# Kernel tuning notes

Hardware: AMD Instinct MI355X
Metric: run time of the kernel (lower is better)

## Reference

```python
import jax, jax.numpy as jnp
import numpy as np

EPS = 1e-5


def _conv1x1(x, w, b):
    # x: (B,C,H,W), w: (O,C), b: (O,)
    return jnp.einsum('bchw,oc->bohw', x, w) + b[None, :, None, None]


def setup_inputs() -> dict:
    key = jax.random.key(0)
    ks = jax.random.split(key, 12)
    C, Ci = 512, 256
    B, H, W = 4, 64, 64
    s_in = 1.0 / np.sqrt(C)
    s_ci = 1.0 / np.sqrt(Ci)
    return {
        'x': jax.random.normal(ks[0], (B, C, H, W), dtype=jnp.float32),
        'g_w': jax.random.normal(ks[1], (Ci, C), dtype=jnp.float32) * s_in,
        'g_b': jax.random.normal(ks[2], (Ci,), dtype=jnp.float32) * 0.01,
        'theta_w': jax.random.normal(ks[3], (Ci, C), dtype=jnp.float32) * s_in,
        'theta_b': jax.random.normal(ks[4], (Ci,), dtype=jnp.float32) * 0.01,
        'phi_w': jax.random.normal(ks[5], (Ci, C), dtype=jnp.float32) * s_in,
        'phi_b': jax.random.normal(ks[6], (Ci,), dtype=jnp.float32) * 0.01,
        'W_w': jax.random.normal(ks[7], (C, Ci), dtype=jnp.float32) * s_ci,
        'W_b': jax.random.normal(ks[8], (C,), dtype=jnp.float32) * 0.01,
        'bn_gamma': jax.random.normal(ks[9], (C,), dtype=jnp.float32) * 0.1,
        'bn_beta': jax.random.normal(ks[10], (C,), dtype=jnp.float32) * 0.01,
    }


def reference(x, g_w, g_b, theta_w, theta_b, phi_w, phi_b, W_w, W_b, bn_gamma, bn_beta):
    B, C, H, W = x.shape
    Ci = g_w.shape[0]
    HW = H * W
    # 1x1-conv projections -> token form
    g = _conv1x1(x, g_w, g_b).reshape(B, Ci, HW).transpose(0, 2, 1)        # (B,HW,Ci)
    theta = _conv1x1(x, theta_w, theta_b).reshape(B, Ci, HW).transpose(0, 2, 1)  # (B,HW,Ci)
    phi = _conv1x1(x, phi_w, phi_b).reshape(B, Ci, HW)                      # (B,Ci,HW)
    # dense HWxHW attention, scaled by sqrt(inter_channels)
    pairwise = jnp.einsum('bnc,bcm->bnm', theta, phi) / jnp.sqrt(jnp.float32(Ci))
    attn = jax.nn.softmax(pairwise, axis=-1)
    y = jnp.einsum('bnm,bmc->bnc', attn, g)                                 # (B,HW,Ci)
    y = y.transpose(0, 2, 1).reshape(B, Ci, H, W)
    # output 1x1 conv + BatchNorm2d (training-mode batch statistics)
    z = _conv1x1(y, W_w, W_b)
    mean = jnp.mean(z, axis=(0, 2, 3), keepdims=True)
    var = jnp.var(z, axis=(0, 2, 3), keepdims=True)
    z = bn_gamma[None, :, None, None] * (z - mean) * jax.lax.rsqrt(var + EPS) + bn_beta[None, :, None, None]
    return z + x
```

## Files before the change

kernel.cpp:

```cpp
#include <hip/hip_runtime.h>

typedef unsigned short u16;
typedef __attribute__((ext_vector_type(4))) u16 u16x4;
typedef __attribute__((ext_vector_type(8))) u16 u16x8;
typedef __attribute__((ext_vector_type(8))) short s16x8;
typedef __attribute__((ext_vector_type(4))) float f32x4;

#define B_  4
#define C_  512
#define CI_ 256
#define HW_ 4096

static __device__ __forceinline__ u16 f2bf(float f) {
  unsigned u = __float_as_uint(f);
  return (u16)((u + 0x7FFFu + ((u >> 16) & 1u)) >> 16);
}
static __device__ __forceinline__ float bf2f(u16 h) {
  return __uint_as_float(((unsigned)h) << 16);
}

static __device__ __forceinline__ f32x4 mfma16(s16x8 a, s16x8 b, f32x4 c) {
  return __builtin_amdgcn_mfma_f32_16x16x32_bf16(a, b, c, 0, 0, 0);
}

typedef __attribute__((address_space(3))) unsigned int as3_u32;
typedef const __attribute__((address_space(1))) unsigned int as1_u32;
static __device__ __forceinline__ void gload16(const u16* g, u16* l) {
  __builtin_amdgcn_global_load_lds((as1_u32*)g, (as3_u32*)l, 16, 0, 0);
}

__global__ __launch_bounds__(256) void k0_wcvt(
    const float* __restrict__ wg, const float* __restrict__ wt,
    const float* __restrict__ wp, const float* __restrict__ Ww,
    u16* __restrict__ wB, u16* __restrict__ WwB)
{
  int idx = (blockIdx.x * 256 + threadIdx.x) * 8;
  const float* src;
  u16* dst;
  if (idx < 393216) {
    int r = idx >> 17;
    src = (r == 0 ? wg : r == 1 ? wt : wp) + (idx & 131071);
    dst = wB + idx;
  } else {
    src = Ww + (idx - 393216);
    dst = WwB + (idx - 393216);
  }
  float4 v0 = *reinterpret_cast<const float4*>(src);
  float4 v1 = *reinterpret_cast<const float4*>(src + 4);
  u16x8 h;
  h[0] = f2bf(v0.x); h[1] = f2bf(v0.y); h[2] = f2bf(v0.z); h[3] = f2bf(v0.w);
  h[4] = f2bf(v1.x); h[5] = f2bf(v1.y); h[6] = f2bf(v1.z); h[7] = f2bf(v1.w);
  *reinterpret_cast<u16x8*>(dst) = h;
}

__global__ __launch_bounds__(256) void k0_xt(
    const float* __restrict__ x, u16* __restrict__ xT, int b0)
{
  __shared__ u16 lds[64][72];
  const int tid = threadIdx.x;
  const int n0 = blockIdx.x * 64, c0 = blockIdx.y * 64;
  const int bl = blockIdx.z;
  const int b = b0 + bl;
  const int nc = (tid & 15) * 4;
#pragma unroll
  for (int i = 0; i < 4; ++i) {
    int cr = (tid >> 4) + i * 16;
    float4 v = *reinterpret_cast<const float4*>(
        &x[((size_t)(b * C_ + c0 + cr)) * HW_ + n0 + nc]);
    u16x4 h; h[0] = f2bf(v.x); h[1] = f2bf(v.y); h[2] = f2bf(v.z); h[3] = f2bf(v.w);
    *reinterpret_cast<u16x4*>(&lds[cr][nc]) = h;
  }
  __syncthreads();
  const int n = tid & 63, cg = tid >> 6;
  u16x8 o0, o1;
#pragma unroll
  for (int j = 0; j < 8; ++j) { o0[j] = lds[cg * 16 + j][n]; o1[j] = lds[cg * 16 + 8 + j][n]; }
  size_t dstb = ((size_t)bl * HW_ + n0 + n) * C_ + c0 + cg * 16;
  *reinterpret_cast<u16x8*>(&xT[dstb])     = o0;
  *reinterpret_cast<u16x8*>(&xT[dstb + 8]) = o1;
}

__global__ __launch_bounds__(256) void k1_proj(
    const u16* __restrict__ wB, const u16* __restrict__ xT,
    const float* __restrict__ bg, const float* __restrict__ bt, const float* __restrict__ bp,
    u16* __restrict__ g_s, u16* __restrict__ thetaT, u16* __restrict__ phiT, int half)
{
  extern __shared__ u16 sm1[];
  const int tid = threadIdx.x;
  const int lane = tid & 63, wid = tid >> 6;
  const int wm = wid >> 1, wn = wid & 1;
  const int l15 = lane & 15, g4 = lane >> 4;

  const int bid = blockIdx.x;
  const int r12 = bid % 12;
  const int nt = bid / 12;
  const int mt = r12 >> 1;
  const int bl = r12 & 1;
  const int b = half * 2 + bl;
  const int m0 = mt * 128, n0g = nt * 128;
  const int p = mt >> 1;

  const u16* xb = xT + (size_t)bl * HW_ * C_;

  const int srow = tid >> 2, sch = tid & 3;
  const u16* a_src = wB + (size_t)(m0 + srow) * C_ + sch * 8;
  const u16* b_src = xb + (size_t)(n0g + srow) * C_ + sch * 8;

  f32x4 acc[4][4] = {};

  auto stage1 = [&](int buf, int ks) {
    u16* d = sm1 + buf * 8192;
#pragma unroll
    for (int i = 0; i < 2; ++i) {
      gload16(a_src + (size_t)(i * 64) * C_ + ks * 32, d + (tid + i * 256) * 8);
      gload16(b_src + (size_t)(i * 64) * C_ + ks * 32, d + 4096 + (tid + i * 256) * 8);
    }
  };
  auto compute1 = [&](int buf) {
    const u16* A = sm1 + buf * 8192;
    const u16* Bt = A + 4096;
    s16x8 afr[4], bfr[4];
#pragma unroll
    for (int mf = 0; mf < 4; ++mf)
      afr[mf] = *reinterpret_cast<const s16x8*>(&A[(wm * 64 + mf * 16 + l15) * 32 + g4 * 8]);
#pragma unroll
    for (int nf = 0; nf < 4; ++nf)
      bfr[nf] = *reinterpret_cast<const s16x8*>(&Bt[(wn * 64 + nf * 16 + l15) * 32 + g4 * 8]);
#pragma unroll
    for (int mf = 0; mf < 4; ++mf)
#pragma unroll
      for (int nf = 0; nf < 4; ++nf)
        acc[mf][nf] = mfma16(afr[mf], bfr[nf], acc[mf][nf]);
  };

  stage1(0, 0); stage1(1, 1);
  int cur = 0;
#pragma unroll 1
  for (int ks = 0; ks < 15; ++ks) {
    asm volatile("s_waitcnt vmcnt(4)" ::: "memory");
    __builtin_amdgcn_s_barrier();
    compute1(cur);
    if (ks < 14) { int nb = cur + 2; if (nb >= 3) nb -= 3; stage1(nb, ks + 2); }
    cur = (cur == 2) ? 0 : cur + 1;
  }
  asm volatile("s_waitcnt vmcnt(0)" ::: "memory");
  __builtin_amdgcn_s_barrier();
  compute1(cur);
  __syncthreads();

  const float* bias = (p == 0) ? bg : (p == 1) ? bt : bp;
  const int cib = (mt & 1) * 128;
#pragma unroll
  for (int mf = 0; mf < 4; ++mf)
#pragma unroll
    for (int r = 0; r < 4; ++r) {
      float bv = bias[cib + wm * 64 + mf * 16 + g4 * 4 + r];
#pragma unroll
      for (int nf = 0; nf < 4; ++nf) acc[mf][nf][r] += bv;
    }

  if (p == 0) {
    u16* lds_t = sm1;
#pragma unroll
    for (int mf = 0; mf < 4; ++mf)
#pragma unroll
      for (int nf = 0; nf < 4; ++nf)
#pragma unroll
        for (int r = 0; r < 4; ++r)
          lds_t[(wm * 64 + mf * 16 + g4 * 4 + r) * 136 + wn * 64 + nf * 16 + l15] =
              f2bf(acc[mf][nf][r]);
    __syncthreads();
    const int m = tid >> 1, hh = tid & 1;
    size_t dst = ((size_t)b * CI_ + cib + m) * HW_ + n0g + hh * 64;
#pragma unroll
    for (int j = 0; j < 8; ++j)
      *reinterpret_cast<u16x8*>(&g_s[dst + j * 8]) =
          *reinterpret_cast<const u16x8*>(&lds_t[m * 136 + hh * 64 + j * 8]);
  } else {
    u16* outp = (p == 1) ? thetaT : phiT;
#pragma unroll
    for (int mf = 0; mf < 4; ++mf)
#pragma unroll
      for (int nf = 0; nf < 4; ++nf) {
        u16x4 h;
#pragma unroll
        for (int r = 0; r < 4; ++r) h[r] = f2bf(acc[mf][nf][r]);
        int n = n0g + wn * 64 + nf * 16 + l15;
        *reinterpret_cast<u16x4*>(
            &outp[((size_t)b * HW_ + n) * CI_ + cib + wm * 64 + mf * 16 + g4 * 4]) = h;
      }
  }
}

#define OFF_PHI  0
#define OFF_G    16384
#define OFF_P    32768
#define OFF_LP   35072

__global__ __launch_bounds__(256, 2) void k3_fused(
    const u16* __restrict__ thetaT, const u16* __restrict__ phiT,
    const u16* __restrict__ g_s, u16* __restrict__ y)
{
  extern __shared__ u16 smem[];
  float* Lp = (float*)(smem + OFF_LP);
  float* iL = Lp + 128;

  const int tid = threadIdx.x;
  const int lane = tid & 63, w = tid >> 6;
  const int l15 = lane & 15, g4 = lane >> 4;

  const int bid = blockIdx.x;
  const int xcd = bid & 7, slot = bid >> 3;
  const int b  = xcd >> 1;
  const int n0 = ((xcd & 1) * 64 + slot) * 32;

  const int ms = w;
  const int cq = w;

  const u16* thb = thetaT + (size_t)b * HW_ * CI_;
  const u16* phb = phiT   + (size_t)b * HW_ * CI_;
  const u16* gsb = g_s    + (size_t)b * CI_ * HW_;

  s16x8 thfr[2][8];
#pragma unroll
  for (int nf = 0; nf < 2; ++nf)
#pragma unroll
    for (int cs = 0; cs < 8; ++cs)
      thfr[nf][cs] = *reinterpret_cast<const s16x8*>(
          &thb[(size_t)(n0 + nf * 16 + l15) * CI_ + cs * 32 + g4 * 8]);

  const int prow = tid >> 5, pj = tid & 31;
  const int grow = tid >> 3, gj = tid & 7;
  const u16* ph_src = phb + (size_t)prow * CI_ + ((pj ^ (prow & 7)) * 8);
  const u16* g_src  = gsb + (size_t)grow * HW_ + ((gj ^ (grow & 7)) * 8);
  const int ph_do = prow * 256 + pj * 8;
  const int g_do  = grow * 64 + gj * 8;

  auto stage_phi = [&](int mt) {
#pragma unroll
    for (int i = 0; i < 8; ++i)
      gload16(ph_src + (size_t)(mt + i * 8) * CI_, smem + OFF_PHI + ph_do + i * 2048);
  };
  auto stage_g = [&](int mt) {
#pragma unroll
    for (int i = 0; i < 8; ++i)
      gload16(g_src + mt + (size_t)i * 32 * HW_, smem + OFF_G + g_do + i * 2048);
  };

  f32x4 oacc[2][4] = {};
  float psum[2] = {0.f, 0.f};

  auto qk_it = [&]() {
    const u16* phc = smem + OFF_PHI;
    u16* pb = smem + OFF_P;
    f32x4 acc[2] = {};
    __builtin_amdgcn_s_setprio(1);
#pragma unroll
    for (int cs = 0; cs < 8; ++cs) {
      s16x8 a = *reinterpret_cast<const s16x8*>(
          &phc[(ms * 16 + l15) * 256 + (((cs * 4 + g4) ^ (l15 & 7)) * 8)]);
      acc[0] = mfma16(a, thfr[0][cs], acc[0]);
      acc[1] = mfma16(a, thfr[1][cs], acc[1]);
    }
    __builtin_amdgcn_s_setprio(0);
#pragma unroll
    for (int nf = 0; nf < 2; ++nf) {
      u16x4 pk;
#pragma unroll
      for (int r = 0; r < 4; ++r) {
        float e = __expf(acc[nf][r] * 0.0625f);
        psum[nf] += e;
        pk[r] = f2bf(e);
      }
      *reinterpret_cast<u16x4*>(&pb[(nf * 16 + l15) * 72 + ms * 16 + g4 * 4]) = pk;
    }
  };
  auto pv_it = [&]() {
    const u16* pb = smem + OFF_P;
    const u16* gC = smem + OFF_G;
    __builtin_amdgcn_s_setprio(1);
#pragma unroll
    for (int mk = 0; mk < 2; ++mk) {
      s16x8 pa[2];
#pragma unroll
      for (int nf = 0; nf < 2; ++nf)
        pa[nf] = *reinterpret_cast<const s16x8*>(
            &pb[(nf * 16 + l15) * 72 + mk * 32 + g4 * 8]);
#pragma unroll
      for (int cf = 0; cf < 4; ++cf) {
        int crow = cq * 64 + cf * 16 + l15;
        s16x8 bb = *reinterpret_cast<const s16x8*>(
            &gC[crow * 64 + (((mk * 4 + g4) ^ (crow & 7)) * 8)]);
        oacc[0][cf] = mfma16(pa[0], bb, oacc[0][cf]);
        oacc[1][cf] = mfma16(pa[1], bb, oacc[1][cf]);
      }
    }
    __builtin_amdgcn_s_setprio(0);
  };

  stage_phi(0);
  __syncthreads();

#pragma unroll 1
  for (int it = 0; it < 64; ++it) {
    stage_g(it * 64);
    qk_it();
    __syncthreads();
    if (it < 63) stage_phi((it + 1) * 64);
    pv_it();
    __syncthreads();
  }

#pragma unroll
  for (int nf = 0; nf < 2; ++nf) {
    psum[nf] += __shfl_xor(psum[nf], 16);
    psum[nf] += __shfl_xor(psum[nf], 32);
  }
  if (lane < 16) {
    Lp[w * 32 + lane]      = psum[0];
    Lp[w * 32 + 16 + lane] = psum[1];
  }
  __syncthreads();
  if (tid < 32) iL[tid] = 1.0f / (Lp[tid] + Lp[32 + tid] + Lp[64 + tid] + Lp[96 + tid]);
  __syncthreads();

  u16* yb = y + ((size_t)b * HW_ + n0) * CI_;
#pragma unroll
  for (int nf = 0; nf < 2; ++nf)
#pragma unroll
    for (int r = 0; r < 4; ++r) {
      int nl = nf * 16 + g4 * 4 + r;
      float il = iL[nl];
#pragma unroll
      for (int cf = 0; cf < 4; ++cf)
        yb[(size_t)nl * CI_ + cq * 64 + cf * 16 + l15] = f2bf(oacc[nf][cf][r] * il);
    }
}

__global__ __launch_bounds__(256) void k4_wconv(
    const u16* __restrict__ WwB, const u16* __restrict__ y, const float* __restrict__ Wb,
    u16* __restrict__ z, float* __restrict__ zsum, float* __restrict__ zsq)
{
  extern __shared__ u16 sm4[];
  __shared__ float lds_ps[2][128][2];
  const int tid = threadIdx.x;
  const int lane = tid & 63, wid = tid >> 6;
  const int wm = wid >> 1, wn = wid & 1;
  const int l15 = lane & 15, g4 = lane >> 4;

  const int bid = blockIdx.x;
  const int xcd = bid & 7, slot = bid >> 3;
  const int b = xcd >> 1, half = xcd & 1;
  const int mt = slot & 3;
  const int nt = half * 16 + (slot >> 2);
  const int o0 = mt * 128, n0g = nt * 128;

  const int srow = tid >> 2, sch = tid & 3;
  const u16* a_src = WwB + (size_t)(o0 + srow) * CI_ + sch * 8;
  const u16* b_src = y + ((size_t)(b * HW_ + n0g + srow)) * CI_ + sch * 8;

  f32x4 acc[4][4] = {};

  auto stage4 = [&](int buf, int ks) {
    u16* d = sm4 + buf * 8192;
#pragma unroll
    for (int i = 0; i < 2; ++i) {
      gload16(a_src + (size_t)(i * 64) * CI_ + ks * 32, d + (tid + i * 256) * 8);
      gload16(b_src + (size_t)(i * 64) * CI_ + ks * 32, d + 4096 + (tid + i * 256) * 8);
    }
  };
  auto compute4 = [&](int buf) {
    const u16* A = sm4 + buf * 8192;
    const u16* Bt = A + 4096;
    s16x8 afr[4], bfr[4];
#pragma unroll
    for (int mf = 0; mf < 4; ++mf)
      afr[mf] = *reinterpret_cast<const s16x8*>(&A[(wm * 64 + mf * 16 + l15) * 32 + g4 * 8]);
#pragma unroll
    for (int nf = 0; nf < 4; ++nf)
      bfr[nf] = *reinterpret_cast<const s16x8*>(&Bt[(wn * 64 + nf * 16 + l15) * 32 + g4 * 8]);
#pragma unroll
    for (int mf = 0; mf < 4; ++mf)
#pragma unroll
      for (int nf = 0; nf < 4; ++nf)
        acc[mf][nf] = mfma16(afr[mf], bfr[nf], acc[mf][nf]);
  };

  stage4(0, 0); stage4(1, 1);
  int cur = 0;
#pragma unroll 1
  for (int ks = 0; ks < 7; ++ks) {
    asm volatile("s_waitcnt vmcnt(4)" ::: "memory");
    __builtin_amdgcn_s_barrier();
    compute4(cur);
    if (ks < 6) { int nb = cur + 2; if (nb >= 3) nb -= 3; stage4(nb, ks + 2); }
    cur = (cur == 2) ? 0 : cur + 1;
  }
  asm volatile("s_waitcnt vmcnt(0)" ::: "memory");
  __builtin_amdgcn_s_barrier();
  compute4(cur);
  __syncthreads();

  u16* lds_t = sm4;
#pragma unroll
  for (int mf = 0; mf < 4; ++mf)
#pragma unroll
    for (int r = 0; r < 4; ++r) {
      const int ol = wm * 64 + mf * 16 + g4 * 4 + r;
      float wb = Wb[o0 + ol];
      float s = 0.f, q = 0.f;
#pragma unroll
      for (int nf = 0; nf < 4; ++nf) {
        float zv = acc[mf][nf][r] + wb;
        s += zv; q += zv * zv;
        lds_t[ol * 136 + wn * 64 + nf * 16 + l15] = f2bf(zv);
      }
      s += __shfl_xor(s, 1); s += __shfl_xor(s, 2); s += __shfl_xor(s, 4); s += __shfl_xor(s, 8);
      q += __shfl_xor(q, 1); q += __shfl_xor(q, 2); q += __shfl_xor(q, 4); q += __shfl_xor(q, 8);
      if (l15 == 0) { lds_ps[wn][ol][0] = s; lds_ps[wn][ol][1] = q; }
    }
  __syncthreads();
  {
    const int m = tid >> 1, hh = tid & 1;
    size_t dst = ((size_t)(b * C_ + o0 + m)) * HW_ + n0g + hh * 64;
#pragma unroll
    for (int j = 0; j < 8; ++j)
      *reinterpret_cast<u16x8*>(&z[dst + j * 8]) =
          *reinterpret_cast<const u16x8*>(&lds_t[m * 136 + hh * 64 + j * 8]);
  }
  if (tid < 128) {
    int col = b * 32 + nt;
    zsum[(size_t)(o0 + tid) * 128 + col] = lds_ps[0][tid][0] + lds_ps[1][tid][0];
    zsq [(size_t)(o0 + tid) * 128 + col] = lds_ps[0][tid][1] + lds_ps[1][tid][1];
  }
}

__global__ void k5_bnstat(const float* __restrict__ zsum, const float* __restrict__ zsq,
                          const float* __restrict__ gamma, const float* __restrict__ beta,
                          float* __restrict__ bns, float* __restrict__ bnb)
{
  int ch = blockIdx.x * 256 + threadIdx.x;
  if (ch >= C_) return;
  float s = 0.f, q = 0.f;
  for (int i = 0; i < 128; ++i) { s += zsum[(size_t)ch * 128 + i]; q += zsq[(size_t)ch * 128 + i]; }
  const float inv_n = 1.0f / (B_ * HW_);
  float mean = s * inv_n;
  float var  = q * inv_n - mean * mean;
  float sc = gamma[ch] * rsqrtf(var + 1e-5f);
  bns[ch] = sc;
  bnb[ch] = beta[ch] - mean * sc;
}

__global__ __launch_bounds__(256) void k6_final(
    const u16* __restrict__ z, const float* __restrict__ x,
    const float* __restrict__ bns, const float* __restrict__ bnb,
    float* __restrict__ out)
{
  size_t i = ((size_t)blockIdx.x * 256 + threadIdx.x) * 8;
  int ch = (int)((i >> 12) & 511);
  float sc = bns[ch], sh = bnb[ch];
  u16x8 zv = *reinterpret_cast<const u16x8*>(&z[i]);
  float4 x0 = *reinterpret_cast<const float4*>(&x[i]);
  float4 x1 = *reinterpret_cast<const float4*>(&x[i + 4]);
  float4 o0, o1;
  o0.x = bf2f(zv[0]) * sc + sh + x0.x;
  o0.y = bf2f(zv[1]) * sc + sh + x0.y;
  o0.z = bf2f(zv[2]) * sc + sh + x0.z;
  o0.w = bf2f(zv[3]) * sc + sh + x0.w;
  o1.x = bf2f(zv[4]) * sc + sh + x1.x;
  o1.y = bf2f(zv[5]) * sc + sh + x1.y;
  o1.z = bf2f(zv[6]) * sc + sh + x1.z;
  o1.w = bf2f(zv[7]) * sc + sh + x1.w;
  *reinterpret_cast<float4*>(&out[i])     = o0;
  *reinterpret_cast<float4*>(&out[i + 4]) = o1;
}

extern "C" void kernel_launch(void* const* d_in, const int* in_sizes, int n_in,
                              void* d_out, int out_size, void* d_ws, size_t ws_size,
                              hipStream_t stream)
{
  (void)in_sizes; (void)n_in; (void)out_size; (void)ws_size;
  const float* x    = (const float*)d_in[0];
  const float* g_w  = (const float*)d_in[1];
  const float* g_b  = (const float*)d_in[2];
  const float* t_w  = (const float*)d_in[3];
  const float* t_b  = (const float*)d_in[4];
  const float* p_w  = (const float*)d_in[5];
  const float* p_b  = (const float*)d_in[6];
  const float* W_w  = (const float*)d_in[7];
  const float* W_b  = (const float*)d_in[8];
  const float* bng  = (const float*)d_in[9];
  const float* bnb_ = (const float*)d_in[10];

  char* ws = (char*)d_ws;
  const size_t M8 = (size_t)8 << 20;
  u16*   xT     = (u16*)(ws + 0);
  u16*   y      = (u16*)(ws + 0);
  u16*   thetaT = (u16*)(ws + M8);
  u16*   phiT   = (u16*)(ws + 2 * M8);
  u16*   g_s    = (u16*)(ws + 3 * M8);
  u16*   zbf    = (u16*)(ws + M8);
  float* zsum   = (float*)(ws + 3 * M8);
  float* zsq    = (float*)(ws + 3 * M8 + 262144);
  float* bnsV   = (float*)(ws + 3 * M8 + 524288);
  float* bnbV   = (float*)(ws + 3 * M8 + 526336);
  u16*   wB     = (u16*)(ws + 4 * M8);
  u16*   WwB    = (u16*)(ws + 4 * M8 + 786432);
  float* out    = (float*)d_out;

  const int k1_lds = 49152;
  const int k3_lds = 70784;
  const int k4_lds = 49152;
  hipFuncSetAttribute(reinterpret_cast<const void*>(k1_proj),
                      hipFuncAttributeMaxDynamicSharedMemorySize, k1_lds);
  hipFuncSetAttribute(reinterpret_cast<const void*>(k3_fused),
                      hipFuncAttributeMaxDynamicSharedMemorySize, k3_lds);
  hipFuncSetAttribute(reinterpret_cast<const void*>(k4_wconv),
                      hipFuncAttributeMaxDynamicSharedMemorySize, k4_lds);

  hipLaunchKernelGGL(k0_wcvt, dim3(256), dim3(256), 0, stream,
                     g_w, t_w, p_w, W_w, wB, WwB);
  for (int half = 0; half < 2; ++half) {
    hipLaunchKernelGGL(k0_xt, dim3(64, 8, 2), dim3(256), 0, stream, x, xT, half * 2);
    hipLaunchKernelGGL(k1_proj, dim3(384), dim3(256), k1_lds, stream,
                       wB, xT, g_b, t_b, p_b, g_s, thetaT, phiT, half);
  }
  hipLaunchKernelGGL(k3_fused, dim3(512), dim3(256), k3_lds, stream,
                     thetaT, phiT, g_s, y);
  hipLaunchKernelGGL(k4_wconv, dim3(512), dim3(256), k4_lds, stream,
                     WwB, y, W_b, zbf, zsum, zsq);
  hipLaunchKernelGGL(k5_bnstat, dim3(2), dim3(256), 0, stream,
                     zsum, zsq, bng, bnb_, bnsV, bnbV);
  hipLaunchKernelGGL(k6_final, dim3(4096), dim3(256), 0, stream,
                     zbf, x, bnsV, bnbV, out);
}
```

Before: 201.6 us.

## Load phi fragments directly into registers with double buffering instead of LDS staging

Result: slower. 283.5 us (+40.6%).

```diff
diff --git a/kernel.cpp b/kernel.cpp
--- a/kernel.cpp
+++ b/kernel.cpp
@@ -192,10 +192,9 @@
   }
 }
 
-#define OFF_PHI  0
-#define OFF_G    16384
-#define OFF_P    32768
-#define OFF_LP   35072
+#define OFF_G    0
+#define OFF_P    16384
+#define OFF_LP   18688
 
 __global__ __launch_bounds__(256, 2) void k3_fused(
     const u16* __restrict__ thetaT, const u16* __restrict__ phiT,
@@ -229,38 +228,35 @@
       thfr[nf][cs] = *reinterpret_cast<const s16x8*>(
           &thb[(size_t)(n0 + nf * 16 + l15) * CI_ + cs * 32 + g4 * 8]);
 
-  const int prow = tid >> 5, pj = tid & 31;
   const int grow = tid >> 3, gj = tid & 7;
-  const u16* ph_src = phb + (size_t)prow * CI_ + ((pj ^ (prow & 7)) * 8);
   const u16* g_src  = gsb + (size_t)grow * HW_ + ((gj ^ (grow & 7)) * 8);
-  const int ph_do = prow * 256 + pj * 8;
   const int g_do  = grow * 64 + gj * 8;
 
-  auto stage_phi = [&](int mt) {
-#pragma unroll
-    for (int i = 0; i < 8; ++i)
-      gload16(ph_src + (size_t)(mt + i * 8) * CI_, smem + OFF_PHI + ph_do + i * 2048);
-  };
   auto stage_g = [&](int mt) {
 #pragma unroll
     for (int i = 0; i < 8; ++i)
       gload16(g_src + mt + (size_t)i * 32 * HW_, smem + OFF_G + g_do + i * 2048);
   };
 
+  const u16* ph_lane = phb + ((size_t)(ms * 16 + l15)) * CI_ + g4 * 8;
+  auto load_phi = [&](s16x8* ph, int mt) {
+    const u16* src = ph_lane + (size_t)mt * CI_;
+#pragma unroll
+    for (int cs = 0; cs < 8; ++cs)
+      ph[cs] = *reinterpret_cast<const s16x8*>(&src[cs * 32]);
+  };
+
   f32x4 oacc[2][4] = {};
   float psum[2] = {0.f, 0.f};
 
-  auto qk_it = [&]() {
-    const u16* phc = smem + OFF_PHI;
+  auto qk_it = [&](const s16x8* ph) {
     u16* pb = smem + OFF_P;
     f32x4 acc[2] = {};
     __builtin_amdgcn_s_setprio(1);
 #pragma unroll
     for (int cs = 0; cs < 8; ++cs) {
-      s16x8 a = *reinterpret_cast<const s16x8*>(
-          &phc[(ms * 16 + l15) * 256 + (((cs * 4 + g4) ^ (l15 & 7)) * 8)]);
-      acc[0] = mfma16(a, thfr[0][cs], acc[0]);
-      acc[1] = mfma16(a, thfr[1][cs], acc[1]);
+      acc[0] = mfma16(ph[cs], thfr[0][cs], acc[0]);
+      acc[1] = mfma16(ph[cs], thfr[1][cs], acc[1]);
     }
     __builtin_amdgcn_s_setprio(0);
 #pragma unroll
@@ -298,15 +294,22 @@
     __builtin_amdgcn_s_setprio(0);
   };
 
-  stage_phi(0);
-  __syncthreads();
+  s16x8 phiA[8], phiB[8];
+
+  load_phi(phiA, 0);
 
 #pragma unroll 1
-  for (int it = 0; it < 64; ++it) {
+  for (int it = 0; it < 64; it += 2) {
+    load_phi(phiB, (it + 1) * 64);
     stage_g(it * 64);
-    qk_it();
+    qk_it(phiA);
     __syncthreads();
-    if (it < 63) stage_phi((it + 1) * 64);
+    pv_it();
+    __syncthreads();
+    if (it + 2 < 64) load_phi(phiA, (it + 2) * 64);
+    stage_g((it + 1) * 64);
+    qk_it(phiB);
+    __syncthreads();
     pv_it();
     __syncthreads();
   }
@@ -509,7 +512,7 @@
   float* out    = (float*)d_out;
 
   const int k1_lds = 49152;
-  const int k3_lds = 70784;
+  const int k3_lds = 38016;
   const int k4_lds = 49152;
   hipFuncSetAttribute(reinterpret_cast<const void*>(k1_proj),
                       hipFuncAttributeMaxDynamicSharedMemorySize, k1_lds);
```

## Retile fused attention kernel to 64-row blocks with 32x32 bf16 MFMA

Applied to the files above, without the earlier changes.

Result: faster. 187.5 us, median of 2 (-7.0%).

```diff
diff --git a/kernel.cpp b/kernel.cpp
--- a/kernel.cpp
+++ b/kernel.cpp
@@ -5,6 +5,7 @@
 typedef __attribute__((ext_vector_type(8))) u16 u16x8;
 typedef __attribute__((ext_vector_type(8))) short s16x8;
 typedef __attribute__((ext_vector_type(4))) float f32x4;
+typedef __attribute__((ext_vector_type(16))) float f32x16;
 
 #define B_  4
 #define C_  512
@@ -21,6 +22,9 @@
 
 static __device__ __forceinline__ f32x4 mfma16(s16x8 a, s16x8 b, f32x4 c) {
   return __builtin_amdgcn_mfma_f32_16x16x32_bf16(a, b, c, 0, 0, 0);
+}
+static __device__ __forceinline__ f32x16 mfma32(s16x8 a, s16x8 b, f32x16 c) {
+  return __builtin_amdgcn_mfma_f32_32x32x16_bf16(a, b, c, 0, 0, 0);
 }
 
 typedef __attribute__((address_space(3))) unsigned int as3_u32;
@@ -193,106 +197,103 @@
 }
 
 #define OFF_PHI  0
-#define OFF_G    16384
-#define OFF_P    32768
-#define OFF_LP   35072
-
-__global__ __launch_bounds__(256, 2) void k3_fused(
+#define OFF_G    32768
+#define OFF_P    65536
+#define OFF_LP   73728
+
+__global__ __launch_bounds__(512, 2) void k3_fused(
     const u16* __restrict__ thetaT, const u16* __restrict__ phiT,
     const u16* __restrict__ g_s, u16* __restrict__ y)
 {
   extern __shared__ u16 smem[];
   float* Lp = (float*)(smem + OFF_LP);
-  float* iL = Lp + 128;
+  float* iL = Lp + 256;
 
   const int tid = threadIdx.x;
   const int lane = tid & 63, w = tid >> 6;
-  const int l15 = lane & 15, g4 = lane >> 4;
+  const int l31 = lane & 31, h = lane >> 5;
+  const int l15 = lane & 15;
 
   const int bid = blockIdx.x;
   const int xcd = bid & 7, slot = bid >> 3;
   const int b  = xcd >> 1;
-  const int n0 = ((xcd & 1) * 64 + slot) * 32;
-
-  const int ms = w;
-  const int cq = w;
+  const int n0 = ((xcd & 1) * 32 + slot) * 64;
+
+  const int mh = w >> 1, nh = w & 1;
+  const int cq = w >> 1, nh2 = w & 1;
 
   const u16* thb = thetaT + (size_t)b * HW_ * CI_;
   const u16* phb = phiT   + (size_t)b * HW_ * CI_;
   const u16* gsb = g_s    + (size_t)b * CI_ * HW_;
 
-  s16x8 thfr[2][8];
-#pragma unroll
-  for (int nf = 0; nf < 2; ++nf)
-#pragma unroll
-    for (int cs = 0; cs < 8; ++cs)
-      thfr[nf][cs] = *reinterpret_cast<const s16x8*>(
-          &thb[(size_t)(n0 + nf * 16 + l15) * CI_ + cs * 32 + g4 * 8]);
+  s16x8 thfr[16];
+#pragma unroll
+  for (int cs = 0; cs < 16; ++cs)
+    thfr[cs] = *reinterpret_cast<const s16x8*>(
+        &thb[(size_t)(n0 + nh * 32 + l31) * CI_ + cs * 16 + h * 8]);
 
   const int prow = tid >> 5, pj = tid & 31;
-  const int grow = tid >> 3, gj = tid & 7;
-  const u16* ph_src = phb + (size_t)prow * CI_ + ((pj ^ (prow & 7)) * 8);
-  const u16* g_src  = gsb + (size_t)grow * HW_ + ((gj ^ (grow & 7)) * 8);
+  const int grow = tid >> 4, gj = tid & 15;
+  const u16* ph_src = phb + (size_t)prow * CI_ + ((pj ^ prow) * 8);
+  const u16* g_src  = gsb + (size_t)grow * HW_ + ((gj ^ (grow & 15)) * 8);
   const int ph_do = prow * 256 + pj * 8;
-  const int g_do  = grow * 64 + gj * 8;
+  const int g_do  = grow * 128 + gj * 8;
 
   auto stage_phi = [&](int mt) {
 #pragma unroll
     for (int i = 0; i < 8; ++i)
-      gload16(ph_src + (size_t)(mt + i * 8) * CI_, smem + OFF_PHI + ph_do + i * 2048);
+      gload16(ph_src + (size_t)(mt + i * 16) * CI_, smem + OFF_PHI + ph_do + i * 4096);
   };
   auto stage_g = [&](int mt) {
 #pragma unroll
     for (int i = 0; i < 8; ++i)
-      gload16(g_src + mt + (size_t)i * 32 * HW_, smem + OFF_G + g_do + i * 2048);
-  };
-
-  f32x4 oacc[2][4] = {};
-  float psum[2] = {0.f, 0.f};
+      gload16(g_src + mt + (size_t)(i * 32) * HW_, smem + OFF_G + g_do + i * 4096);
+  };
+
+  f32x16 oacc[2] = {};
+  float psum = 0.f;
 
   auto qk_it = [&]() {
     const u16* phc = smem + OFF_PHI;
     u16* pb = smem + OFF_P;
-    f32x4 acc[2] = {};
+    f32x16 acc = {};
     __builtin_amdgcn_s_setprio(1);
 #pragma unroll
-    for (int cs = 0; cs < 8; ++cs) {
+    for (int cs = 0; cs < 16; ++cs) {
       s16x8 a = *reinterpret_cast<const s16x8*>(
-          &phc[(ms * 16 + l15) * 256 + (((cs * 4 + g4) ^ (l15 & 7)) * 8)]);
-      acc[0] = mfma16(a, thfr[0][cs], acc[0]);
-      acc[1] = mfma16(a, thfr[1][cs], acc[1]);
+          &phc[(mh * 32 + l31) * 256 + (((cs * 2 + h) ^ l15) * 8)]);
+      acc = mfma32(a, thfr[cs], acc);
     }
     __builtin_amdgcn_s_setprio(0);
-#pragma unroll
-    for (int nf = 0; nf < 2; ++nf) {
+    const int nloc = nh * 32 + l31;
+#pragma unroll
+    for (int g = 0; g < 4; ++g) {
       u16x4 pk;
 #pragma unroll
       for (int r = 0; r < 4; ++r) {
-        float e = __expf(acc[nf][r] * 0.0625f);
-        psum[nf] += e;
+        float e = __expf(acc[4 * g + r] * 0.0625f);
+        psum += e;
         pk[r] = f2bf(e);
       }
-      *reinterpret_cast<u16x4*>(&pb[(nf * 16 + l15) * 72 + ms * 16 + g4 * 4]) = pk;
+      *reinterpret_cast<u16x4*>(
+          &pb[nloc * 128 + (((mh * 4 + g) ^ l15) * 8) + h * 4]) = pk;
     }
   };
   auto pv_it = [&]() {
     const u16* pb = smem + OFF_P;
     const u16* gC = smem + OFF_G;
+    const int nloc = nh2 * 32 + l31;
     __builtin_amdgcn_s_setprio(1);
 #pragma unroll
-    for (int mk = 0; mk < 2; ++mk) {
-      s16x8 pa[2];
-#pragma unroll
-      for (int nf = 0; nf < 2; ++nf)
-        pa[nf] = *reinterpret_cast<const s16x8*>(
-            &pb[(nf * 16 + l15) * 72 + mk * 32 + g4 * 8]);
-#pragma unroll
-      for (int cf = 0; cf < 4; ++cf) {
-        int crow = cq * 64 + cf * 16 + l15;
-        s16x8 bb = *reinterpret_cast<const s16x8*>(
-            &gC[crow * 64 + (((mk * 4 + g4) ^ (crow & 7)) * 8)]);
-        oacc[0][cf] = mfma16(pa[0], bb, oacc[0][cf]);
-        oacc[1][cf] = mfma16(pa[1], bb, oacc[1][cf]);
+    for (int ks = 0; ks < 8; ++ks) {
+      s16x8 pa = *reinterpret_cast<const s16x8*>(
+          &pb[nloc * 128 + (((ks * 2 + h) ^ l15) * 8)]);
+#pragma unroll
+      for (int ct = 0; ct < 2; ++ct) {
+        int c = cq * 64 + ct * 32 + l31;
+        s16x8 gb = *reinterpret_cast<const s16x8*>(
+            &gC[c * 128 + (((ks * 2 + h) ^ l15) * 8)]);
+        oacc[ct] = mfma32(pa, gb, oacc[ct]);
       }
     }
     __builtin_amdgcn_s_setprio(0);
@@ -302,39 +303,35 @@
   __syncthreads();
 
 #pragma unroll 1
-  for (int it = 0; it < 64; ++it) {
-    stage_g(it * 64);
+  for (int it = 0; it < 32; ++it) {
+    stage_g(it * 128);
     qk_it();
     __syncthreads();
-    if (it < 63) stage_phi((it + 1) * 64);
+    if (it < 31) stage_phi((it + 1) * 128);
     pv_it();
     __syncthreads();
   }
 
-#pragma unroll
-  for (int nf = 0; nf < 2; ++nf) {
-    psum[nf] += __shfl_xor(psum[nf], 16);
-    psum[nf] += __shfl_xor(psum[nf], 32);
-  }
-  if (lane < 16) {
-    Lp[w * 32 + lane]      = psum[0];
-    Lp[w * 32 + 16 + lane] = psum[1];
-  }
-  __syncthreads();
-  if (tid < 32) iL[tid] = 1.0f / (Lp[tid] + Lp[32 + tid] + Lp[64 + tid] + Lp[96 + tid]);
+  psum += __shfl_xor(psum, 32);
+  if (lane < 32) Lp[w * 32 + lane] = psum;
+  __syncthreads();
+  if (tid < 64) {
+    int nhh = tid >> 5, j = tid & 31;
+    iL[tid] = 1.0f / (Lp[(0 * 2 + nhh) * 32 + j] + Lp[(1 * 2 + nhh) * 32 + j] +
+                      Lp[(2 * 2 + nhh) * 32 + j] + Lp[(3 * 2 + nhh) * 32 + j]);
+  }
   __syncthreads();
 
   u16* yb = y + ((size_t)b * HW_ + n0) * CI_;
 #pragma unroll
-  for (int nf = 0; nf < 2; ++nf)
-#pragma unroll
-    for (int r = 0; r < 4; ++r) {
-      int nl = nf * 16 + g4 * 4 + r;
-      float il = iL[nl];
-#pragma unroll
-      for (int cf = 0; cf < 4; ++cf)
-        yb[(size_t)nl * CI_ + cq * 64 + cf * 16 + l15] = f2bf(oacc[nf][cf][r] * il);
-    }
+  for (int ct = 0; ct < 2; ++ct) {
+    int c = cq * 64 + ct * 32 + l31;
+#pragma unroll
+    for (int reg = 0; reg < 16; ++reg) {
+      int nl = nh2 * 32 + (reg & 3) + 8 * (reg >> 2) + 4 * h;
+      yb[(size_t)nl * CI_ + c] = f2bf(oacc[ct][reg] * iL[nl]);
+    }
+  }
 }
 
 __global__ __launch_bounds__(256) void k4_wconv(
@@ -509,7 +506,7 @@
   float* out    = (float*)d_out;
 
   const int k1_lds = 49152;
-  const int k3_lds = 70784;
+  const int k3_lds = 148736;
   const int k4_lds = 49152;
   hipFuncSetAttribute(reinterpret_cast<const void*>(k1_proj),
                       hipFuncAttributeMaxDynamicSharedMemorySize, k1_lds);
@@ -525,7 +522,7 @@
     hipLaunchKernelGGL(k1_proj, dim3(384), dim3(256), k1_lds, stream,
                        wB, xT, g_b, t_b, p_b, g_s, thetaT, phiT, half);
   }
-  hipLaunchKernelGGL(k3_fused, dim3(512), dim3(256), k3_lds, stream,
+  hipLaunchKernelGGL(k3_fused, dim3(256), dim3(512), k3_lds, stream,
                      thetaT, phiT, g_s, y);
   hipLaunchKernelGGL(k4_wconv, dim3(512), dim3(256), k4_lds, stream,
                      WwB, y, W_b, zbf, zsum, zsq);
```
